# Kernel tuning notes

Hardware: AMD Instinct MI355X
Metric: run time of the kernel (lower is better)

Reference implementation:

```python
import jax, jax.numpy as jnp
import numpy as np
import math

B, T, DIM, NH = 2, 2048, 2048, 16
HD = DIM // NH  # 128


def rotate_half(x):
    h = x.shape[-1] // 2
    return jnp.concatenate([-x[..., h:], x[..., :h]], axis=-1)


def rope_tables(t_len, rot_dim, base=10000.0, dtype=jnp.float32):
    # rot_dim = head_dim; inv_freq has rot_dim//2 entries -> sin/cos [T, rot_dim//2]
    inv_freq = 1.0 / (base ** (jnp.arange(0, rot_dim, 2, dtype=dtype) / rot_dim))
    t = jnp.arange(t_len, dtype=dtype)
    ang = jnp.einsum('i,j->ij', t, inv_freq)  # [T, rot_dim//2]
    return jnp.sin(ang), jnp.cos(ang)


def apply_rope(q, k, sin, cos):
    # Partial RoPE as in source: rotate only the first half of head_dim,
    # using sin/cos of width head_dim//2 matched to that half.
    h = q.shape[-1] // 2
    q1, q2 = q[..., :h], q[..., h:]
    k1, k2 = k[..., :h], k[..., h:]
    sin = sin[None, None]  # [1,1,T,h]
    cos = cos[None, None]
    q1r = q1 * cos + rotate_half(q1) * sin
    k1r = k1 * cos + rotate_half(k1) * sin
    return jnp.concatenate([q1r, q2], axis=-1), jnp.concatenate([k1r, k2], axis=-1)


def setup_inputs() -> dict:
    key = jax.random.key(0)
    ks = jax.random.split(key, 5)
    s = 1.0 / math.sqrt(DIM)
    return {
        'x': jax.random.normal(ks[0], (B, T, DIM), jnp.float32),
        'wq': jax.random.normal(ks[1], (DIM, DIM), jnp.float32) * s,
        'wk': jax.random.normal(ks[2], (DIM, DIM), jnp.float32) * s,
        'wv': jax.random.normal(ks[3], (DIM, DIM), jnp.float32) * s,
        'wo': jax.random.normal(ks[4], (DIM, DIM), jnp.float32) * s,
    }


def reference(x, wq, wk, wv, wo):
    b, t, c = x.shape
    def proj(w):
        return (x @ w.T).reshape(b, t, NH, HD).transpose(0, 2, 1, 3)  # [B,H,T,hd]
    q, k, v = proj(wq), proj(wk), proj(wv)
    sin, cos = rope_tables(t, HD, dtype=x.dtype)
    q, k = apply_rope(q, k, sin, cos)
    att = jnp.einsum('bhqd,bhkd->bhqk', q, k) * (1.0 / math.sqrt(HD))  # [B,H,T,T]
    att = jax.nn.softmax(att, axis=-1)
    y = jnp.einsum('bhqk,bhkd->bhqd', att, v)
    y = y.transpose(0, 2, 1, 3).reshape(b, t, c)
    return y @ wo.T
```

## Files before the change

kernel.cpp:

```cpp
#include <hip/hip_runtime.h>

typedef unsigned short u16;
typedef __attribute__((ext_vector_type(4))) u16 u16x4;
typedef __attribute__((ext_vector_type(8))) __bf16 bf16x8;
typedef __attribute__((ext_vector_type(4))) float f32x4;

#define B_ 2
#define T_ 2048
#define DIM_ 2048
#define NH_ 16
#define HD_ 128

__device__ __forceinline__ u16 f2b(float f) {
  unsigned u = __builtin_bit_cast(unsigned, f);
  u += 0x7fffu + ((u >> 16) & 1u);
  return (u16)(u >> 16);
}
__device__ __forceinline__ float b2f(u16 h) {
  unsigned u = ((unsigned)h) << 16;
  return __builtin_bit_cast(float, u);
}
__device__ __forceinline__ unsigned pack2(float lo, float hi) {
  return (unsigned)f2b(lo) | ((unsigned)f2b(hi) << 16);
}

typedef __attribute__((address_space(1))) void gvoid_t;
typedef __attribute__((address_space(3))) void lvoid_t;
__device__ __forceinline__ void gload16(const void* g, void* l) {
  __builtin_amdgcn_global_load_lds((gvoid_t*)g, (lvoid_t*)l, 16, 0, 0);
}

__global__ __launch_bounds__(256) void cvt_bf16(const float* x, const float* wq,
    const float* wk, const float* wv, const float* wo,
    u16* xb, u16* wqb, u16* wkb, u16* wvb, u16* wob) {
  int ten = blockIdx.y;
  const float* s; u16* d; int n4;
  if (ten == 0)      { s = x;  d = xb;  n4 = 2097152; }
  else if (ten == 1) { s = wq; d = wqb; n4 = 1048576; }
  else if (ten == 2) { s = wk; d = wkb; n4 = 1048576; }
  else if (ten == 3) { s = wv; d = wvb; n4 = 1048576; }
  else               { s = wo; d = wob; n4 = 1048576; }
  int i = blockIdx.x * 256 + threadIdx.x;
  if (i >= n4) return;
  float4 f = ((const float4*)s)[i];
  u16x4 o = { f2b(f.x), f2b(f.y), f2b(f.z), f2b(f.w) };
  ((u16x4*)d)[i] = o;
}

template <typename OutT>
__device__ __forceinline__ void gemm_bt_body(const u16* A, const u16* Bw, OutT* C) {
  constexpr int K = 2048, N = 2048;
  __shared__ u16 As[128 * 32];
  __shared__ u16 Bs[128 * 32];
  const int tid = threadIdx.x;
  const int w = tid >> 6, l = tid & 63, n = l & 15, quad = l >> 4;
  const int row0 = blockIdx.y * 128, col0 = blockIdx.x * 128;
  const int c = w * 64 + l;
  const int rA = c >> 2, kA = (c & 3) * 8;
  const u16* aP1 = A + (size_t)(row0 + rA) * K + kA;
  const u16* aP2 = A + (size_t)(row0 + 64 + rA) * K + kA;
  const u16* bP1 = Bw + (size_t)(col0 + rA) * K + kA;
  const u16* bP2 = Bw + (size_t)(col0 + 64 + rA) * K + kA;
  char* lA1 = (char*)As + (w * 64) * 16;
  char* lA2 = (char*)As + (256 + w * 64) * 16;
  char* lB1 = (char*)Bs + (w * 64) * 16;
  char* lB2 = (char*)Bs + (256 + w * 64) * 16;
  const int wr0 = (w >> 1) * 64, wc0 = (w & 1) * 64;
  f32x4 acc[4][4] = {};
  for (int kt = 0; kt < K; kt += 32) {
    gload16(aP1, lA1); gload16(aP2, lA2);
    gload16(bP1, lB1); gload16(bP2, lB2);
    aP1 += 32; aP2 += 32; bP1 += 32; bP2 += 32;
    __syncthreads();
    bf16x8 af[4], bfr[4];
#pragma unroll
    for (int mb = 0; mb < 4; ++mb)
      af[mb] = *(const bf16x8*)&As[(wr0 + mb * 16 + n) * 32 + quad * 8];
#pragma unroll
    for (int nb = 0; nb < 4; ++nb)
      bfr[nb] = *(const bf16x8*)&Bs[(wc0 + nb * 16 + n) * 32 + quad * 8];
#pragma unroll
    for (int mb = 0; mb < 4; ++mb)
#pragma unroll
      for (int nb = 0; nb < 4; ++nb)
        acc[mb][nb] = __builtin_amdgcn_mfma_f32_16x16x32_bf16(af[mb], bfr[nb], acc[mb][nb], 0, 0, 0);
    __syncthreads();
  }
#pragma unroll
  for (int mb = 0; mb < 4; ++mb)
#pragma unroll
    for (int nb = 0; nb < 4; ++nb)
#pragma unroll
      for (int r = 0; r < 4; ++r) {
        size_t idx = (size_t)(row0 + wr0 + mb * 16 + quad * 4 + r) * N + (col0 + wc0 + nb * 16 + n);
        float v = acc[mb][nb][r];
        if constexpr (sizeof(OutT) == 2) C[idx] = f2b(v); else C[idx] = v;
      }
}

__global__ __launch_bounds__(256) void gemm_qkv(const u16* A, const u16* w0, const u16* w1,
    const u16* w2, u16* c0, u16* c1, u16* c2) {
  const u16* Bw = (blockIdx.z == 0) ? w0 : (blockIdx.z == 1) ? w1 : w2;
  u16* C = (blockIdx.z == 0) ? c0 : (blockIdx.z == 1) ? c1 : c2;
  gemm_bt_body<u16>(A, Bw, C);
}
__global__ __launch_bounds__(256) void gemm_o(const u16* A, const u16* Bw, float* C) {
  gemm_bt_body<float>(A, Bw, C);
}

__global__ __launch_bounds__(256) void rope_k(u16* Qb, u16* Kb) {
  int gid = blockIdx.x * 256 + threadIdx.x;
  int j = gid & 31;
  int h = (gid >> 5) & 15;
  int row = gid >> 9;
  int t = row & (T_ - 1);
  bool isQ = (blockIdx.y == 0);
  u16* base = (isQ ? Qb : Kb) + (size_t)row * DIM_ + h * HD_;
  double f1 = exp2(-(double)j * 0.20762050593045951);
  double f2 = f1 * 0.01;
  const double INV2PI = 0.15915494309189535;
  double r1d = (double)t * f1 * INV2PI; r1d -= floor(r1d);
  double r2d = (double)t * f2 * INV2PI; r2d -= floor(r2d);
  float rv1 = (float)r1d, rv2 = (float)r2d;
  float c1 = __builtin_amdgcn_cosf(rv1), s1 = __builtin_amdgcn_sinf(rv1);
  float c2 = __builtin_amdgcn_cosf(rv2), s2 = __builtin_amdgcn_sinf(rv2);
  float x1 = b2f(base[j]), x2 = b2f(base[j + 32]);
  float scale = isQ ? 0.12751743342408354f : 1.0f;
  base[j]      = f2b((x1 * c1 - x2 * s1) * scale);
  base[j + 32] = f2b((x2 * c2 + x1 * s2) * scale);
  if (isQ) {
    base[j + 64] = f2b(b2f(base[j + 64]) * scale);
    base[j + 96] = f2b(b2f(base[j + 96]) * scale);
  }
}

__global__ __launch_bounds__(256) void transpose_v(const u16* V, u16* Vt) {
  int b = blockIdx.z;
  int t0 = blockIdx.x * 64, c0 = blockIdx.y * 64;
  __shared__ u16 tile[64][72];
  int tid = threadIdx.x;
#pragma unroll
  for (int i = 0; i < 4; ++i) {
    int v = i * 256 + tid;
    int r = v >> 4, c4 = (v & 15) * 4;
    *(u16x4*)&tile[r][c4] = *(const u16x4*)(V + (size_t)(b * T_ + t0 + r) * DIM_ + c0 + c4);
  }
  __syncthreads();
#pragma unroll
  for (int i = 0; i < 4; ++i) {
    int v = i * 256 + tid;
    int d = v >> 4, t4 = (v & 15) * 4;
    u16x4 o = { tile[t4 + 0][d], tile[t4 + 1][d], tile[t4 + 2][d], tile[t4 + 3][d] };
    *(u16x4*)(Vt + (size_t)(b * DIM_ + c0 + d) * T_ + t0 + t4) = o;
  }
}

__global__ __launch_bounds__(256, 2) void attn_k(const u16* Q, const u16* K, const u16* Vt, u16* Y) {
  const int qt = blockIdx.x, bh = blockIdx.y;
  const int b = bh >> 4, h = bh & 15;
  const int tid = threadIdx.x;
  const int w = tid >> 6, l = tid & 63, n = l & 15, quad = l >> 4;
  __shared__ u16 Ks[128 * 128];
  __shared__ u16 Vs[128 * 128];

  const u16* Qbase = Q + (size_t)(b * T_ + qt * 128 + w * 32) * DIM_ + h * HD_;
  const u16* Kbase = K + (size_t)(b * T_) * DIM_ + h * HD_;
  const u16* Vbase = Vt + (size_t)(b * DIM_ + h * HD_) * T_;

  bf16x8 qf[2][4];
#pragma unroll
  for (int qtile = 0; qtile < 2; ++qtile)
#pragma unroll
    for (int ks = 0; ks < 4; ++ks)
      qf[qtile][ks] = *(const bf16x8*)(Qbase + (size_t)(qtile * 16 + n) * DIM_ + ks * 32 + quad * 8);

  auto stage = [&](const u16* rowbase, u16* lds) {
#pragma unroll
    for (int inst = 0; inst < 8; ++inst) {
      int ci = inst * 256 + w * 64 + l;
      int r = ci >> 4, cl = ci & 15;
      int cg = cl ^ (4 * (r & 3));
      gload16(rowbase + (size_t)r * 2048 + cg * 8, (char*)lds + (inst * 256 + w * 64) * 16);
    }
  };

  stage(Kbase, Ks);
  stage(Vbase, Vs);

  f32x4 o[2][8] = {};
  float m_r[2] = { -__builtin_inff(), -__builtin_inff() };
  float l_r[2] = { 0.f, 0.f };

  const int shA = ((quad & 1) * 2) * 16 + n;
  const int shB = shA + 16;
  const bool hiTile = (quad >= 2);

  for (int it = 0; it < 16; ++it) {
    __syncthreads();

    f32x4 st[2][8] = {};
#pragma unroll
    for (int ks = 0; ks < 4; ++ks) {
      bf16x8 kf[8];
#pragma unroll
      for (int mt = 0; mt < 8; ++mt)
        kf[mt] = *(const bf16x8*)&Ks[(mt * 16 + n) * 128 + (((ks * 4 + quad) ^ (4 * (n & 3))) * 8)];
#pragma unroll
      for (int qtile = 0; qtile < 2; ++qtile)
#pragma unroll
        for (int mt = 0; mt < 8; ++mt)
          st[qtile][mt] = __builtin_amdgcn_mfma_f32_16x16x32_bf16(kf[mt], qf[qtile][ks], st[qtile][mt], 0, 0, 0);
    }
    __syncthreads();
    if (it + 1 < 16) stage(Kbase + (size_t)((it + 1) * 128) * 2048, Ks);

    unsigned pk[2][8][2];
#pragma unroll
    for (int qtile = 0; qtile < 2; ++qtile) {
      float mx = -__builtin_inff();
#pragma unroll
      for (int mt = 0; mt < 8; ++mt)
#pragma unroll
        for (int r = 0; r < 4; ++r) mx = fmaxf(mx, st[qtile][mt][r]);
      mx = fmaxf(mx, __shfl_xor(mx, 16, 64));
      mx = fmaxf(mx, __shfl_xor(mx, 32, 64));
      float mo = m_r[qtile];
      float mn = fmaxf(mo, mx);
      float al = __builtin_amdgcn_exp2f(mo - mn);
      float rs = 0.f;
#pragma unroll
      for (int mt = 0; mt < 8; ++mt)
#pragma unroll
        for (int r = 0; r < 4; ++r) {
          float p = __builtin_amdgcn_exp2f(st[qtile][mt][r] - mn);
          st[qtile][mt][r] = p;
          rs += p;
        }
      rs += __shfl_xor(rs, 16, 64);
      rs += __shfl_xor(rs, 32, 64);
      l_r[qtile] = al * l_r[qtile] + rs;
      m_r[qtile] = mn;
#pragma unroll
      for (int mt = 0; mt < 8; ++mt) {
        pk[qtile][mt][0] = pack2(st[qtile][mt][0], st[qtile][mt][1]);
        pk[qtile][mt][1] = pack2(st[qtile][mt][2], st[qtile][mt][3]);
      }
#pragma unroll
      for (int mt = 0; mt < 8; ++mt)
#pragma unroll
        for (int r = 0; r < 4; ++r) o[qtile][mt][r] *= al;
    }

    typedef __attribute__((ext_vector_type(4))) unsigned uint4v;
    uint4v pT[2][4];
#pragma unroll
    for (int qtile = 0; qtile < 2; ++qtile)
#pragma unroll
      for (int ks = 0; ks < 4; ++ks) {
#pragma unroll
        for (int jj = 0; jj < 4; ++jj) {
          int src = (jj < 2) ? shA : shB;
          unsigned vA = __shfl((int)pk[qtile][ks * 2][jj & 1], src, 64);
          unsigned vB = __shfl((int)pk[qtile][ks * 2 + 1][jj & 1], src, 64);
          pT[qtile][ks][jj] = hiTile ? vB : vA;
        }
      }

#pragma unroll
    for (int ks = 0; ks < 4; ++ks) {
      bf16x8 vf[8];
#pragma unroll
      for (int mt = 0; mt < 8; ++mt)
        vf[mt] = *(const bf16x8*)&Vs[(mt * 16 + n) * 128 + (((ks * 4 + quad) ^ (4 * (n & 3))) * 8)];
#pragma unroll
      for (int qtile = 0; qtile < 2; ++qtile) {
        bf16x8 pfrag = __builtin_bit_cast(bf16x8, pT[qtile][ks]);
#pragma unroll
        for (int mt = 0; mt < 8; ++mt)
          o[qtile][mt] = __builtin_amdgcn_mfma_f32_16x16x32_bf16(vf[mt], pfrag, o[qtile][mt], 0, 0, 0);
      }
    }
    __syncthreads();
    if (it + 1 < 16) stage(Vbase + (it + 1) * 128, Vs);
  }

  u16* Ybase = Y + (size_t)(b * T_ + qt * 128 + w * 32) * DIM_ + h * HD_;
#pragma unroll
  for (int qtile = 0; qtile < 2; ++qtile) {
    float inv = 1.0f / l_r[qtile];
#pragma unroll
    for (int mt = 0; mt < 8; ++mt) {
      u16x4 ov = { f2b(o[qtile][mt][0] * inv), f2b(o[qtile][mt][1] * inv),
                   f2b(o[qtile][mt][2] * inv), f2b(o[qtile][mt][3] * inv) };
      *(u16x4*)(Ybase + (size_t)(qtile * 16 + n) * DIM_ + mt * 16 + quad * 4) = ov;
    }
  }
}

extern "C" void kernel_launch(void* const* d_in, const int* in_sizes, int n_in,
                              void* d_out, int out_size, void* d_ws, size_t ws_size,
                              hipStream_t stream) {
  const float* x  = (const float*)d_in[0];
  const float* wq = (const float*)d_in[1];
  const float* wk = (const float*)d_in[2];
  const float* wv = (const float*)d_in[3];
  const float* wo = (const float*)d_in[4];

  u16* ws  = (u16*)d_ws;
  u16* xb  = ws;
  u16* wqb = xb + 8388608;
  u16* wkb = wqb + 4194304;
  u16* wvb = wkb + 4194304;
  u16* wob = wvb + 4194304;
  u16* qb  = wob + 4194304;
  u16* kb  = qb + 8388608;
  u16* vb  = kb + 8388608;
  u16* vt  = vb + 8388608;
  u16* yb  = vt + 8388608;

  cvt_bf16<<<dim3(8192, 5), 256, 0, stream>>>(x, wq, wk, wv, wo, xb, wqb, wkb, wvb, wob);
  gemm_qkv<<<dim3(16, 32, 3), 256, 0, stream>>>(xb, wqb, wkb, wvb, qb, kb, vb);
  rope_k<<<dim3(8192, 2), 256, 0, stream>>>(qb, kb);
  transpose_v<<<dim3(32, 32, 2), 256, 0, stream>>>(vb, vt);
  attn_k<<<dim3(16, 32), 256, 0, stream>>>(qb, kb, vt, yb);
  gemm_o<<<dim3(16, 32), 256, 0, stream>>>(yb, wob, (float*)d_out);
}
```

Baseline: 441.2 us.

## Double-buffer K/V tiles with 64-key blocks in attention kernel

The attention kernel now processes 64 keys per iteration instead of 128 and keeps two LDS buffers each for K and V. The next tile's async loads are issued at the start of each iteration so they overlap the current tile's compute. This replaces the two mid-iteration barriers and restage points with a single barrier per iteration, and changes the XOR swizzle to suit the new row widths. LDS use stays the same, but softmax rescaling and barriers now run twice as often per key, and smaller MFMA batches per barrier may expose more latency.

```diff
diff --git a/kernel.cpp b/kernel.cpp
--- a/kernel.cpp
+++ b/kernel.cpp
@@ -160,8 +160,8 @@
   const int b = bh >> 4, h = bh & 15;
   const int tid = threadIdx.x;
   const int w = tid >> 6, l = tid & 63, n = l & 15, quad = l >> 4;
-  __shared__ u16 Ks[128 * 128];
-  __shared__ u16 Vs[128 * 128];
+  __shared__ u16 Ks[2][64 * 128];
+  __shared__ u16 Vs[2][128 * 64];
 
   const u16* Qbase = Q + (size_t)(b * T_ + qt * 128 + w * 32) * DIM_ + h * HD_;
   const u16* Kbase = K + (size_t)(b * T_) * DIM_ + h * HD_;
@@ -174,18 +174,24 @@
     for (int ks = 0; ks < 4; ++ks)
       qf[qtile][ks] = *(const bf16x8*)(Qbase + (size_t)(qtile * 16 + n) * DIM_ + ks * 32 + quad * 8);
 
-  auto stage = [&](const u16* rowbase, u16* lds) {
-#pragma unroll
-    for (int inst = 0; inst < 8; ++inst) {
+  auto stageK = [&](int itn, u16* dst) {
+#pragma unroll
+    for (int inst = 0; inst < 4; ++inst) {
       int ci = inst * 256 + w * 64 + l;
       int r = ci >> 4, cl = ci & 15;
-      int cg = cl ^ (4 * (r & 3));
-      gload16(rowbase + (size_t)r * 2048 + cg * 8, (char*)lds + (inst * 256 + w * 64) * 16);
+      int cg = cl ^ (r & 7);
+      gload16(Kbase + (size_t)(itn * 64 + r) * DIM_ + cg * 8, (char*)dst + (inst * 256 + w * 64) * 16);
     }
   };
-
-  stage(Kbase, Ks);
-  stage(Vbase, Vs);
+  auto stageV = [&](int itn, u16* dst) {
+#pragma unroll
+    for (int inst = 0; inst < 4; ++inst) {
+      int ci = inst * 256 + w * 64 + l;
+      int r = ci >> 3, cl = ci & 7;
+      int cg = cl ^ (r & 7);
+      gload16(Vbase + (size_t)r * T_ + itn * 64 + cg * 8, (char*)dst + (inst * 256 + w * 64) * 16);
+    }
+  };
 
   f32x4 o[2][8] = {};
   float m_r[2] = { -__builtin_inff(), -__builtin_inff() };
@@ -195,31 +201,30 @@
   const int shB = shA + 16;
   const bool hiTile = (quad >= 2);
 
-  for (int it = 0; it < 16; ++it) {
+  auto iter_body = [&](const u16* Kc, const u16* Vc, u16* Kn, u16* Vn, int itn) {
     __syncthreads();
-
-    f32x4 st[2][8] = {};
+    if (itn >= 0) { stageK(itn, Kn); stageV(itn, Vn); }
+
+    f32x4 st[2][4] = {};
 #pragma unroll
     for (int ks = 0; ks < 4; ++ks) {
-      bf16x8 kf[8];
-#pragma unroll
-      for (int mt = 0; mt < 8; ++mt)
-        kf[mt] = *(const bf16x8*)&Ks[(mt * 16 + n) * 128 + (((ks * 4 + quad) ^ (4 * (n & 3))) * 8)];
+      bf16x8 kf[4];
+#pragma unroll
+      for (int mt = 0; mt < 4; ++mt)
+        kf[mt] = *(const bf16x8*)&Kc[(mt * 16 + n) * 128 + (((ks * 4 + quad) ^ (n & 7)) * 8)];
 #pragma unroll
       for (int qtile = 0; qtile < 2; ++qtile)
 #pragma unroll
-        for (int mt = 0; mt < 8; ++mt)
+        for (int mt = 0; mt < 4; ++mt)
           st[qtile][mt] = __builtin_amdgcn_mfma_f32_16x16x32_bf16(kf[mt], qf[qtile][ks], st[qtile][mt], 0, 0, 0);
     }
-    __syncthreads();
-    if (it + 1 < 16) stage(Kbase + (size_t)((it + 1) * 128) * 2048, Ks);
-
-    unsigned pk[2][8][2];
+
+    unsigned pk[2][4][2];
 #pragma unroll
     for (int qtile = 0; qtile < 2; ++qtile) {
       float mx = -__builtin_inff();
 #pragma unroll
-      for (int mt = 0; mt < 8; ++mt)
+      for (int mt = 0; mt < 4; ++mt)
 #pragma unroll
         for (int r = 0; r < 4; ++r) mx = fmaxf(mx, st[qtile][mt][r]);
       mx = fmaxf(mx, __shfl_xor(mx, 16, 64));
@@ -229,7 +234,7 @@
       float al = __builtin_amdgcn_exp2f(mo - mn);
       float rs = 0.f;
 #pragma unroll
-      for (int mt = 0; mt < 8; ++mt)
+      for (int mt = 0; mt < 4; ++mt)
 #pragma unroll
         for (int r = 0; r < 4; ++r) {
           float p = __builtin_amdgcn_exp2f(st[qtile][mt][r] - mn);
@@ -241,7 +246,7 @@
       l_r[qtile] = al * l_r[qtile] + rs;
       m_r[qtile] = mn;
 #pragma unroll
-      for (int mt = 0; mt < 8; ++mt) {
+      for (int mt = 0; mt < 4; ++mt) {
         pk[qtile][mt][0] = pack2(st[qtile][mt][0], st[qtile][mt][1]);
         pk[qtile][mt][1] = pack2(st[qtile][mt][2], st[qtile][mt][3]);
       }
@@ -252,36 +257,39 @@
     }
 
     typedef __attribute__((ext_vector_type(4))) unsigned uint4v;
-    uint4v pT[2][4];
+    uint4v pT[2][2];
 #pragma unroll
     for (int qtile = 0; qtile < 2; ++qtile)
 #pragma unroll
-      for (int ks = 0; ks < 4; ++ks) {
+      for (int ks2 = 0; ks2 < 2; ++ks2)
 #pragma unroll
         for (int jj = 0; jj < 4; ++jj) {
           int src = (jj < 2) ? shA : shB;
-          unsigned vA = __shfl((int)pk[qtile][ks * 2][jj & 1], src, 64);
-          unsigned vB = __shfl((int)pk[qtile][ks * 2 + 1][jj & 1], src, 64);
-          pT[qtile][ks][jj] = hiTile ? vB : vA;
+          unsigned vA = __shfl((int)pk[qtile][ks2 * 2][jj & 1], src, 64);
+          unsigned vB = __shfl((int)pk[qtile][ks2 * 2 + 1][jj & 1], src, 64);
+          pT[qtile][ks2][jj] = hiTile ? vB : vA;
         }
-      }
-
-#pragma unroll
-    for (int ks = 0; ks < 4; ++ks) {
+
+#pragma unroll
+    for (int ks2 = 0; ks2 < 2; ++ks2) {
       bf16x8 vf[8];
 #pragma unroll
       for (int mt = 0; mt < 8; ++mt)
-        vf[mt] = *(const bf16x8*)&Vs[(mt * 16 + n) * 128 + (((ks * 4 + quad) ^ (4 * (n & 3))) * 8)];
+        vf[mt] = *(const bf16x8*)&Vc[(mt * 16 + n) * 64 + (((ks2 * 4 + quad) ^ (n & 7)) * 8)];
 #pragma unroll
       for (int qtile = 0; qtile < 2; ++qtile) {
-        bf16x8 pfrag = __builtin_bit_cast(bf16x8, pT[qtile][ks]);
+        bf16x8 pfrag = __builtin_bit_cast(bf16x8, pT[qtile][ks2]);
 #pragma unroll
         for (int mt = 0; mt < 8; ++mt)
           o[qtile][mt] = __builtin_amdgcn_mfma_f32_16x16x32_bf16(vf[mt], pfrag, o[qtile][mt], 0, 0, 0);
       }
     }
-    __syncthreads();
-    if (it + 1 < 16) stage(Vbase + (it + 1) * 128, Vs);
+  };
+
+  stageK(0, Ks[0]); stageV(0, Vs[0]);
+  for (int it = 0; it < 32; it += 2) {
+    iter_body(Ks[0], Vs[0], Ks[1], Vs[1], it + 1);
+    iter_body(Ks[1], Vs[1], Ks[0], Vs[0], (it + 2 < 32) ? it + 2 : -1);
   }
 
   u16* Ybase = Y + (size_t)(b * T_ + qt * 128 + w * 32) * DIM_ + h * HD_;
```

Result: faster. 419.9 us (-4.8%).
